# Kernel tuning notes

Measured on AMD Instinct MI355X. Metric: run time of the kernel, lower is better.

## Reference

```python
import jax, jax.numpy as jnp
import numpy as np

B, N, C = 8, 1024, 768      # batch, tokens, dim
H, HD = 8, 96               # num_heads (= top-k experts per token), head_dim
E, T = 24, 9                # num_experts, task_num
SCALE = HD ** -0.5
W_SWITCH, W_Z = 0.1, 0.001  # switchloss, zloss weights from __init__ defaults


def setup_inputs() -> dict:
    key = jax.random.key(0)
    ks = jax.random.split(key, 5)
    g = lambda k, sh, sc: jax.random.normal(k, sh, dtype=jnp.float32) * sc
    return {
        "x": g(ks[0], (B, N, C), 1.0),
        "W_gate": g(ks[1], (T, C, E), C ** -0.5),   # per-task gating weights
        "W_in": g(ks[2], (E, C, HD), C ** -0.5),    # expert q projections (TaskMoE.map)
        "W_out": g(ks[3], (E, HD, C), HD ** -0.5),  # expert output projections (TaskMoE.reduce)
        "W_kv": g(ks[4], (C, 2 * HD), C ** -0.5),   # shared kv_proj (MQA-style)
        "task_bh": 3,
    }


def reference(x, W_gate, W_in, W_out, W_kv, task_bh):
    # ---- task-conditioned top-k gating (eval path: no noise, no sampling) ----
    logits = jnp.einsum('bnc,ce->bne', x, W_gate[task_bh])          # [B,N,E]
    probs = jax.nn.softmax(logits, axis=-1)
    top_g, top_i = jax.lax.top_k(probs, H)                          # [B,N,H]
    top_g = top_g / (jnp.sum(top_g, axis=-1, keepdims=True) + 1e-6)
    # ---- TaskMoE.map: per-head q = selected expert projection of x ----
    q_all = jnp.einsum('bnc,ecd->bned', x, W_in)                    # [B,N,E,HD]
    q = jnp.take_along_axis(q_all, top_i[..., None], axis=2)        # [B,N,H,HD]
    # ---- shared K/V (single head) ----
    kv = x @ W_kv                                                   # [B,N,2*HD]
    k, v = kv[..., :HD], kv[..., HD:]
    # ---- MQA attention ----
    attn = jnp.einsum('bihd,bjd->bhij', q, k) * SCALE               # [B,H,N,N]
    attn = jax.nn.softmax(attn, axis=-1)
    o = jnp.einsum('bhij,bjd->bihd', attn, v)                       # [B,N,H,HD]
    # ---- TaskMoE.reduce: gate-weighted combine through output experts ----
    onehot = jax.nn.one_hot(top_i, E, dtype=o.dtype)                # [B,N,H,E]
    z = jnp.einsum('bnhd,bnhe,bnh->bned', o, onehot, top_g)         # [B,N,E,HD]
    out = jnp.einsum('bned,edc->bnc', z, W_out)                     # [B,N,C]
    # ---- auxiliary routing losses (switch load-balance + z-loss) ----
    importance = probs.mean(axis=(0, 1))                            # [E]
    load = onehot.sum(axis=2).mean(axis=(0, 1)) / H                 # [E]
    switchloss = E * jnp.sum(importance * load)
    zloss = jnp.mean(jax.nn.logsumexp(logits, axis=-1) ** 2)
    aux_loss = W_SWITCH * switchloss + W_Z * zloss
    return out, aux_loss
```

## Files before the change

kernel.cpp:

```cpp
#include <hip/hip_runtime.h>
#include <hip/hip_bf16.h>
#include <math.h>

#define BB 8
#define NN 1024
#define CC 768
#define HH 8
#define HD 96
#define EE 24
#define NT (BB*NN)
#define NSLOT (NT*HH)
#define EC (EE*HD)
#define CAPQ 8192
#define ASCALE 0.10206207261596575f
#define AL2 0.14724446f
#define DEFER_THR 11.5415603f

typedef unsigned short u16;
typedef unsigned char u8;
typedef unsigned int u32;
typedef unsigned long long u64;
typedef __attribute__((ext_vector_type(8))) short s16x8;
typedef __attribute__((ext_vector_type(4))) float f32x4;
typedef __attribute__((ext_vector_type(16))) float f32x16;

__device__ __forceinline__ u16 f2b(float f) {
  unsigned u = __builtin_bit_cast(unsigned, f);
  unsigned r = u + 0x7fffu + ((u >> 16) & 1u);
  return (u16)(r >> 16);
}

__device__ __forceinline__ float fexp2(float x) {
  float r; asm("v_exp_f32 %0, %1" : "=v"(r) : "v"(x)); return r;
}

__device__ __forceinline__ u32 cvtpk(float a, float b) {
  u32 d; asm("v_cvt_pk_bf16_f32 %0, %1, %2" : "=v"(d) : "v"(a), "v"(b)); return d;
}

__device__ __forceinline__ void gload16(const u16* g, u16* lds) {
  __builtin_amdgcn_global_load_lds(
      (const __attribute__((address_space(1))) void*)g,
      (__attribute__((address_space(3))) void*)lds, 16, 0, 0);
}

__device__ __forceinline__ int xcd_remap(int bid, int nwg) {
  int q = nwg >> 3, r = nwg & 7;
  int xcd = bid & 7, idx = bid >> 3;
  return (xcd < r ? xcd * (q + 1) : r * (q + 1) + (xcd - r) * q) + idx;
}

#define WS_CNT   0
#define WS_IMP   96
#define WS_ZSUM  192
#define WS_G     256
#define WS_EID   (WS_G + NSLOT*4)
#define WS_KVK   (WS_EID + NSLOT)
#define WS_VT    (WS_KVK + NT*128*2)
#define WS_WIN   (WS_VT + (size_t)96*NT*2)
#define WS_WOUT  (WS_WIN + (size_t)EC*CC*2)
#define WS_WKV   (WS_WOUT + (size_t)CC*EC*2)
#define WS_QA    (WS_WKV + 192*CC*2)
#define WS_Z     (WS_QA + (size_t)NT*EC*2)
#define WS_XB    WS_Z
#define WS_BUCKET (WS_Z + (size_t)16*1024*1024)

__global__ __launch_bounds__(256) void gate_kernel(
    const float* __restrict__ x, const float* __restrict__ Wg_all,
    const int* __restrict__ task_p, float* __restrict__ ws_f,
    int* __restrict__ ws_i, u8* __restrict__ eids, u16* __restrict__ xb,
    int* __restrict__ bucket)
{
  __shared__ float xs[64][65];
  __shared__ float wgs[64][24];
  __shared__ float lgt[64][26];
  __shared__ float zlo[64];
  __shared__ int hist[EE];
  __shared__ int gbase[EE];

  int t = threadIdx.x;
  int w = t >> 6, r = t & 63;
  int e0 = w * 6;
  int tok0 = blockIdx.x * 64;
  const float* Wg = Wg_all + (size_t)task_p[0] * CC * EE;

  if (t < EE) hist[t] = 0;

  float acc[6];
  #pragma unroll
  for (int c = 0; c < 6; c++) acc[c] = 0.f;

  for (int kb = 0; kb < CC; kb += 64) {
    __syncthreads();
    #pragma unroll
    for (int i = 0; i < 4; i++) {
      int idx = i * 256 + t;
      int rr = idx >> 4, cc = (idx & 15) << 2;
      float4 v = *(const float4*)&x[(size_t)(tok0 + rr) * CC + kb + cc];
      *(float4*)&xs[rr][cc] = v;
      u64 pk = (u64)f2b(v.x) | ((u64)f2b(v.y) << 16) |
               ((u64)f2b(v.z) << 32) | ((u64)f2b(v.w) << 48);
      *(u64*)&xb[(size_t)(tok0 + rr) * CC + kb + cc] = pk;
    }
    #pragma unroll
    for (int i = 0; i < 3; i++) {
      int idx = i * 256 + t;
      int kk = idx / 12, c2 = idx % 12;
      *(float2*)&wgs[kk][c2 * 2] = *(const float2*)&Wg[(size_t)(kb + kk) * EE + c2 * 2];
    }
    __syncthreads();
    #pragma unroll 16
    for (int k = 0; k < 64; k++) {
      float xv = xs[r][k];
      float2 w01 = *(const float2*)&wgs[k][e0];
      float2 w23 = *(const float2*)&wgs[k][e0 + 2];
      float2 w45 = *(const float2*)&wgs[k][e0 + 4];
      acc[0] += xv * w01.x; acc[1] += xv * w01.y;
      acc[2] += xv * w23.x; acc[3] += xv * w23.y;
      acc[4] += xv * w45.x; acc[5] += xv * w45.y;
    }
  }
  __syncthreads();
  #pragma unroll
  for (int c = 0; c < 6; c++) lgt[r][e0 + c] = acc[c];
  __syncthreads();

  int my_e[8], loc[8];
  if (t < 64) {
    int token = tok0 + t;
    float l[EE];
    #pragma unroll
    for (int e = 0; e < EE; e++) l[e] = lgt[t][e];
    float mx = l[0];
    #pragma unroll
    for (int e = 1; e < EE; e++) mx = fmaxf(mx, l[e]);
    float se = 0.f; float probs[EE];
    #pragma unroll
    for (int e = 0; e < EE; e++) { probs[e] = __expf(l[e] - mx); se += probs[e]; }
    float inv = 1.f / se;
    #pragma unroll
    for (int e = 0; e < EE; e++) probs[e] *= inv;
    float lse = mx + __logf(se);
    zlo[t] = lse * lse;

    unsigned taken = 0u;
    float gsum = 0.f;
    float my_g[8];
    #pragma unroll
    for (int h = 0; h < HH; h++) {
      float best = -1.f; int bi = 0;
      #pragma unroll
      for (int e = 0; e < EE; e++) {
        bool ok = !((taken >> e) & 1u) && (probs[e] > best);
        best = ok ? probs[e] : best;
        bi   = ok ? e : bi;
      }
      taken |= 1u << bi;
      gsum += best;
      my_g[h] = best; my_e[h] = bi;
    }
    float ginv = 1.f / (gsum + 1e-6f);
    float4 g0, g1;
    g0.x = my_g[0] * ginv; g0.y = my_g[1] * ginv; g0.z = my_g[2] * ginv; g0.w = my_g[3] * ginv;
    g1.x = my_g[4] * ginv; g1.y = my_g[5] * ginv; g1.z = my_g[6] * ginv; g1.w = my_g[7] * ginv;
    float* gbuf = ws_f + WS_G / 4;
    *(float4*)&gbuf[(size_t)token * HH]     = g0;
    *(float4*)&gbuf[(size_t)token * HH + 4] = g1;
    u64 pk = 0;
    #pragma unroll
    for (int h = 0; h < HH; h++) pk |= (u64)(u8)my_e[h] << (8 * h);
    *(u64*)&eids[(size_t)token * HH] = pk;
    #pragma unroll
    for (int h = 0; h < HH; h++) loc[h] = atomicAdd(&hist[my_e[h]], 1);
    #pragma unroll
    for (int e = 0; e < EE; e++) lgt[t][e] = probs[e];
  }
  __syncthreads();
  if (t < EE) {
    float s = 0.f;
    #pragma unroll 8
    for (int rr = 0; rr < 64; rr++) s += lgt[rr][t];
    atomicAdd(ws_f + WS_IMP / 4 + t, s);
    gbase[t] = atomicAdd(&ws_i[t], hist[t]);
  } else if (t == 32) {
    float s = 0.f;
    #pragma unroll 8
    for (int rr = 0; rr < 64; rr++) s += zlo[rr];
    atomicAdd(ws_f + WS_ZSUM / 4, s);
  }
  __syncthreads();
  if (t < 64) {
    int token = tok0 + t;
    #pragma unroll
    for (int h = 0; h < HH; h++)
      bucket[my_e[h] * CAPQ + gbase[my_e[h]] + loc[h]] = token;
  }
}

__global__ __launch_bounds__(256) void transpose_kernel(
    const float* __restrict__ src, u16* __restrict__ dst,
    int R, int C, int sB, int dR, int dB)
{
  __shared__ float tile[32][33];
  int e = blockIdx.z;
  const float* s = src + (size_t)e * sB;
  int t = threadIdx.x;
  int tr = t >> 5, tc = t & 31;
  #pragma unroll
  for (int i = 0; i < 4; i++) {
    int r = blockIdx.x * 32 + tr + i * 8;
    int c = blockIdx.y * 32 + tc;
    tile[tr + i * 8][tc] = s[(size_t)r * C + c];
  }
  __syncthreads();
  #pragma unroll
  for (int i = 0; i < 4; i++) {
    int sc = blockIdx.y * 32 + tr + i * 8;
    int sr = blockIdx.x * 32 + tc;
    dst[(size_t)e * dB + (size_t)sc * dR + sr] = f2b(tile[tc][tr + i * 8]);
  }
}

template<int BM, int BN, bool OUT_F32>
__global__ __launch_bounds__(256) void gemm_kernel(
    const u16* __restrict__ A, const u16* __restrict__ Bt,
    void* __restrict__ Cp, int M, int N, int K)
{
  constexpr int WM = BM / 2, WN = BN / 2;
  constexpr int FM = WM / 16, FN = WN / 16;
  __shared__ u16 As[BM][64];
  __shared__ u16 Bs[BN][64];
  int t = threadIdx.x;
  int w = t >> 6, l = t & 63;
  int lr = l & 15, lg = l >> 4;
  int wr = w >> 1, wc = w & 1;
  int nwg = gridDim.x * gridDim.y;
  int logical = xcd_remap(blockIdx.y * gridDim.x + blockIdx.x, nwg);
  int col0 = (logical % gridDim.x) * BN, row0 = (logical / gridDim.x) * BM;

  f32x4 acc[FM][FN];
  #pragma unroll
  for (int i = 0; i < FM; i++)
    #pragma unroll
    for (int j = 0; j < FN; j++) acc[i][j] = (f32x4)(0.f);

  int sr = t >> 3;
  int sc = t & 7;
  for (int kb = 0; kb < K; kb += 64) {
    __syncthreads();
    #pragma unroll
    for (int i = 0; i < BM / 32; i++) {
      int rr = i * 32 + sr;
      int ch = sc ^ (rr & 7);
      gload16(A + (size_t)(row0 + rr) * K + kb + ch * 8, &As[rr][sc * 8]);
    }
    #pragma unroll
    for (int i = 0; i < BN / 32; i++) {
      int rr = i * 32 + sr;
      int ch = sc ^ (rr & 7);
      gload16(Bt + (size_t)(col0 + rr) * K + kb + ch * 8, &Bs[rr][sc * 8]);
    }
    __syncthreads();
    #pragma unroll
    for (int ks = 0; ks < 2; ks++) {
      s16x8 af[FM], bf[FN];
      #pragma unroll
      for (int i = 0; i < FM; i++)
        af[i] = *(const s16x8*)&As[wr * WM + i * 16 + lr][8 * ((ks * 4 + lg) ^ (lr & 7))];
      #pragma unroll
      for (int j = 0; j < FN; j++)
        bf[j] = *(const s16x8*)&Bs[wc * WN + j * 16 + lr][8 * ((ks * 4 + lg) ^ (lr & 7))];
      #pragma unroll
      for (int i = 0; i < FM; i++)
        #pragma unroll
        for (int j = 0; j < FN; j++)
          acc[i][j] = __builtin_amdgcn_mfma_f32_16x16x32_bf16(af[i], bf[j], acc[i][j], 0, 0, 0);
    }
  }
  #pragma unroll
  for (int i = 0; i < FM; i++)
    #pragma unroll
    for (int j = 0; j < FN; j++)
      #pragma unroll
      for (int reg = 0; reg < 4; reg++) {
        int rr = row0 + wr * WM + i * 16 + lg * 4 + reg;
        int cc = col0 + wc * WN + j * 16 + lr;
        if (OUT_F32) ((float*)Cp)[(size_t)rr * N + cc] = acc[i][j][reg];
        else ((u16*)Cp)[(size_t)rr * N + cc] = f2b(acc[i][j][reg]);
      }
}

__global__ __launch_bounds__(256) void qproj_kernel(
    const u16* __restrict__ xb, const u16* __restrict__ winT,
    const int* __restrict__ ws_i, const int* __restrict__ bucket,
    u16* __restrict__ qall)
{
  int e = blockIdx.y;
  int t0 = blockIdx.x * 128;
  int cnt = ws_i[e];
  if (t0 >= cnt) return;
  __shared__ u16 As[128][64];
  __shared__ u16 Bs[96][64];
  __shared__ int tok_s[128];
  int t = threadIdx.x;
  if (t < 128) tok_s[t] = bucket[e * CAPQ + min(t0 + t, cnt - 1)];
  __syncthreads();
  int w = t >> 6, l = t & 63;
  int lr = l & 15, lg = l >> 4;
  int wr = w >> 1, wc = w & 1;
  const u16* Bt = winT + (size_t)e * HD * CC;

  f32x4 acc[4][3];
  #pragma unroll
  for (int i = 0; i < 4; i++)
    #pragma unroll
    for (int j = 0; j < 3; j++) acc[i][j] = (f32x4)(0.f);

  int sr = t >> 3, sc = t & 7;
  int atok[4];
  #pragma unroll
  for (int i = 0; i < 4; i++) atok[i] = tok_s[i * 32 + sr];

  for (int kb = 0; kb < CC; kb += 64) {
    __syncthreads();
    #pragma unroll
    for (int i = 0; i < 4; i++) {
      int rr = i * 32 + sr;
      int ch = sc ^ (rr & 7);
      gload16(xb + (size_t)atok[i] * CC + kb + ch * 8, &As[rr][sc * 8]);
    }
    #pragma unroll
    for (int i = 0; i < 3; i++) {
      int rr = i * 32 + sr;
      int ch = sc ^ (rr & 7);
      gload16(Bt + (size_t)rr * CC + kb + ch * 8, &Bs[rr][sc * 8]);
    }
    __syncthreads();
    #pragma unroll
    for (int ks = 0; ks < 2; ks++) {
      s16x8 af[4], bf[3];
      #pragma unroll
      for (int i = 0; i < 4; i++)
        af[i] = *(const s16x8*)&As[wr * 64 + i * 16 + lr][8 * ((ks * 4 + lg) ^ (lr & 7))];
      #pragma unroll
      for (int j = 0; j < 3; j++)
        bf[j] = *(const s16x8*)&Bs[wc * 48 + j * 16 + lr][8 * ((ks * 4 + lg) ^ (lr & 7))];
      #pragma unroll
      for (int i = 0; i < 4; i++)
        #pragma unroll
        for (int j = 0; j < 3; j++)
          acc[i][j] = __builtin_amdgcn_mfma_f32_16x16x32_bf16(af[i], bf[j], acc[i][j], 0, 0, 0);
    }
  }
  #pragma unroll
  for (int i = 0; i < 4; i++)
    #pragma unroll
    for (int reg = 0; reg < 4; reg++) {
      int rr = wr * 64 + i * 16 + lg * 4 + reg;
      if (t0 + rr < cnt) {
        int tok = tok_s[rr];
        u16* qp = qall + (size_t)tok * EC + e * HD + wc * 48;
        #pragma unroll
        for (int j = 0; j < 3; j++)
          qp[j * 16 + lr] = f2b(acc[i][j][reg]);
      }
    }
}

__global__ __launch_bounds__(256) void kvproj_kernel(
    const u16* __restrict__ xb, const u16* __restrict__ wkvT,
    u16* __restrict__ kvbk, u16* __restrict__ vtb)
{
  __shared__ u16 As[128][64];
  __shared__ u16 Bs[64][64];
  int t = threadIdx.x;
  int w = t >> 6, l = t & 63;
  int lr = l & 15, lg = l >> 4;
  int wr = w >> 1, wc = w & 1;
  int nwg = gridDim.x * gridDim.y;
  int logical = xcd_remap(blockIdx.y * gridDim.x + blockIdx.x, nwg);
  int col0 = (logical % gridDim.x) * 64, row0 = (logical / gridDim.x) * 128;

  f32x4 acc[4][2];
  #pragma unroll
  for (int i = 0; i < 4; i++)
    #pragma unroll
    for (int j = 0; j < 2; j++) acc[i][j] = (f32x4)(0.f);

  int sr = t >> 3, sc = t & 7;
  for (int kb = 0; kb < CC; kb += 64) {
    __syncthreads();
    #pragma unroll
    for (int i = 0; i < 4; i++) {
      int rr = i * 32 + sr;
      int ch = sc ^ (rr & 7);
      gload16(xb + (size_t)(row0 + rr) * CC + kb + ch * 8, &As[rr][sc * 8]);
    }
    #pragma unroll
    for (int i = 0; i < 2; i++) {
      int rr = i * 32 + sr;
      int ch = sc ^ (rr & 7);
      gload16(wkvT + (size_t)(col0 + rr) * CC + kb + ch * 8, &Bs[rr][sc * 8]);
    }
    __syncthreads();
    #pragma unroll
    for (int ks = 0; ks < 2; ks++) {
      s16x8 af[4], bf[2];
      #pragma unroll
      for (int i = 0; i < 4; i++)
        af[i] = *(const s16x8*)&As[wr * 64 + i * 16 + lr][8 * ((ks * 4 + lg) ^ (lr & 7))];
      #pragma unroll
      for (int j = 0; j < 2; j++)
        bf[j] = *(const s16x8*)&Bs[wc * 32 + j * 16 + lr][8 * ((ks * 4 + lg) ^ (lr & 7))];
      #pragma unroll
      for (int i = 0; i < 4; i++)
        #pragma unroll
        for (int j = 0; j < 2; j++)
          acc[i][j] = __builtin_amdgcn_mfma_f32_16x16x32_bf16(af[i], bf[j], acc[i][j], 0, 0, 0);
    }
  }
  #pragma unroll
  for (int i = 0; i < 4; i++)
    #pragma unroll
    for (int j = 0; j < 2; j++) {
      int cb = col0 + wc * 32 + j * 16 + lr;
      int rb = row0 + wr * 64 + i * 16 + lg * 4;
      if (cb < 96) {
        int ch = cb >> 3, ci = cb & 7;
        #pragma unroll
        for (int reg = 0; reg < 4; reg++) {
          int tok = rb + reg;
          kvbk[(size_t)tok * 128 + 8 * (ch ^ (tok & 7)) + ci] = f2b(acc[i][j][reg]);
        }
      } else {
        int d = cb - 96;
        u64 pk = (u64)f2b(acc[i][j][0]) | ((u64)f2b(acc[i][j][1]) << 16) |
                 ((u64)f2b(acc[i][j][2]) << 32) | ((u64)f2b(acc[i][j][3]) << 48);
        int blkbase = rb & ~63;
        int ch = (rb & 63) >> 3;
        *(u64*)&vtb[(size_t)d * NT + blkbase + 8 * (ch ^ (d & 7)) + (rb & 7)] = pk;
      }
    }
}

__global__ __launch_bounds__(256, 2) void attn_kernel(
    const u16* __restrict__ qall, const u16* __restrict__ kvbk,
    const u16* __restrict__ vtb, const u8* __restrict__ eids,
    const float* __restrict__ gbuf, u16* __restrict__ z)
{
  __shared__ u16 Ks[2][64][128];
  __shared__ u16 Vt[2][96][64];
  int b = blockIdx.y;
  int tok0 = blockIdx.x * 32;
  int t = threadIdx.x;
  int w = t >> 6, l = t & 63;
  int h = blockIdx.z * 4 + w;
  int lo = l & 31, hi = l >> 5;

  s16x8 qf[6];
  {
    int tok = b * NN + tok0 + lo;
    int e = eids[tok * HH + h];
    const u16* qp = qall + (size_t)tok * EC + e * HD + hi * 8;
    #pragma unroll
    for (int ks = 0; ks < 6; ks++)
      qf[ks] = *(const s16x8*)(qp + ks * 16);
  }

  const u16* kvwin = kvbk + (size_t)(b * NN) * 128;
  const u16* vwin  = vtb + (size_t)(b * NN);

  f32x16 o0 = (f32x16)(0.f), o1 = (f32x16)(0.f), o2 = (f32x16)(0.f);
  float m = -1e30f, lsum = 0.f;

  #pragma unroll
  for (int k2 = 0; k2 < 4; k2++) {
    int c = t + k2 * 256;
    gload16(kvwin + c * 8, &Ks[0][0][0] + c * 8);
  }
  #pragma unroll
  for (int k2 = 0; k2 < 3; k2++) {
    int c = t + k2 * 256;
    gload16(vwin + (size_t)(c >> 3) * NT + (c & 7) * 8, &Vt[0][0][0] + c * 8);
  }

  for (int jt = 0; jt < 16; jt++) {
    __syncthreads();
    if (jt < 15) {
      int j0 = (jt + 1) * 64;
      int nb = (jt + 1) & 1;
      const u16* kb_ = kvwin + (size_t)j0 * 128;
      #pragma unroll
      for (int k2 = 0; k2 < 4; k2++) {
        int c = t + k2 * 256;
        gload16(kb_ + c * 8, &Ks[nb][0][0] + c * 8);
      }
      const u16* vb_ = vwin + j0;
      #pragma unroll
      for (int k2 = 0; k2 < 3; k2++) {
        int c = t + k2 * 256;
        gload16(vb_ + (size_t)(c >> 3) * NT + (c & 7) * 8, &Vt[nb][0][0] + c * 8);
      }
    }
    int buf = jt & 1;

    f32x16 s0 = (f32x16)(0.f), s1 = (f32x16)(0.f);
    #pragma unroll
    for (int ks = 0; ks < 6; ks++) {
      int pos = 8 * ((2 * ks + hi) ^ (lo & 7));
      s16x8 a0 = *(const s16x8*)&Ks[buf][lo][pos];
      s16x8 a1 = *(const s16x8*)&Ks[buf][32 + lo][pos];
      s0 = __builtin_amdgcn_mfma_f32_32x32x16_bf16(a0, qf[ks], s0, 0, 0, 0);
      s1 = __builtin_amdgcn_mfma_f32_32x32x16_bf16(a1, qf[ks], s1, 0, 0, 0);
    }

    float pm = fmaxf(s0[0], s0[1]);
    #pragma unroll
    for (int rg = 2; rg < 16; rg += 2) pm = fmaxf(pm, fmaxf(s0[rg], s0[rg + 1]));
    #pragma unroll
    for (int rg = 0; rg < 16; rg += 2) pm = fmaxf(pm, fmaxf(s1[rg], s1[rg + 1]));
    pm = fmaxf(pm, __shfl_xor(pm, 32));
    pm *= AL2;

    if (!__all(pm - m <= DEFER_THR)) {
      float mn = fmaxf(m, pm);
      float al = fexp2(m - mn);
      m = mn; lsum *= al;
      #pragma unroll
      for (int rg = 0; rg < 16; rg++) {
        int qrow = (rg & 3) + 8 * (rg >> 2) + 4 * hi;
        float alr = __shfl(al, qrow);
        o0[rg] *= alr; o1[rg] *= alr; o2[rg] *= alr;
      }
    }

    float ts = 0.f;
    u32 wpk[2][4][2];
    #pragma unroll
    for (int kb2 = 0; kb2 < 2; kb2++)
      #pragma unroll
      for (int rr = 0; rr < 4; rr++)
        #pragma unroll
        for (int pp = 0; pp < 2; pp++) {
          float sA = kb2 ? s1[rr * 4 + 2 * pp]     : s0[rr * 4 + 2 * pp];
          float sB = kb2 ? s1[rr * 4 + 2 * pp + 1] : s0[rr * 4 + 2 * pp + 1];
          float eA = fexp2(fmaf(sA, AL2, -m));
          float eB = fexp2(fmaf(sB, AL2, -m));
          ts += eA + eB;
          wpk[kb2][rr][pp] = cvtpk(eA, eB);
        }
    lsum += ts;

    s16x8 pa[4];
    #pragma unroll
    for (int ks = 0; ks < 4; ks++) {
      int kb2 = ks >> 1;
      int rlo = (ks & 1) * 2, rhi = rlo + 1;
      u32 own_lo0 = wpk[kb2][rlo][0], own_lo1 = wpk[kb2][rlo][1];
      u32 own_hi0 = wpk[kb2][rhi][0], own_hi1 = wpk[kb2][rhi][1];
      u32 send0 = hi ? own_lo0 : own_hi0;
      u32 send1 = hi ? own_lo1 : own_hi1;
      u32 recv0 = (u32)__shfl_xor((int)send0, 32);
      u32 recv1 = (u32)__shfl_xor((int)send1, 32);
      union { s16x8 v; u32 u[4]; } pu;
      pu.u[0] = hi ? recv0 : own_lo0;
      pu.u[1] = hi ? recv1 : own_lo1;
      pu.u[2] = hi ? own_hi0 : recv0;
      pu.u[3] = hi ? own_hi1 : recv1;
      pa[ks] = pu.v;
    }

    #pragma unroll
    for (int ks = 0; ks < 4; ks++) {
      int pos = 8 * ((2 * ks + hi) ^ (lo & 7));
      s16x8 v0 = *(const s16x8*)&Vt[buf][lo][pos];
      s16x8 v1 = *(const s16x8*)&Vt[buf][32 + lo][pos];
      s16x8 v2 = *(const s16x8*)&Vt[buf][64 + lo][pos];
      o0 = __builtin_amdgcn_mfma_f32_32x32x16_bf16(pa[ks], v0, o0, 0, 0, 0);
      o1 = __builtin_amdgcn_mfma_f32_32x32x16_bf16(pa[ks], v1, o1, 0, 0, 0);
      o2 = __builtin_amdgcn_mfma_f32_32x32x16_bf16(pa[ks], v2, o2, 0, 0, 0);
    }
  }

  float lt = lsum + __shfl_xor(lsum, 32);
  #pragma unroll
  for (int rg = 0; rg < 16; rg++) {
    int qrow = (rg & 3) + 8 * (rg >> 2) + 4 * hi;
    float lv = __shfl(lt, qrow);
    int tok = b * NN + tok0 + qrow;
    int slot = tok * HH + h;
    float scl = gbuf[slot] / lv;
    int e = eids[slot];
    u16* zp = z + (size_t)tok * EC + e * HD + lo;
    zp[0]  = f2b(o0[rg] * scl);
    zp[32] = f2b(o1[rg] * scl);
    zp[64] = f2b(o2[rg] * scl);
  }
}

__global__ void aux_kernel(const float* __restrict__ ws_f,
                           const int* __restrict__ ws_i, float* __restrict__ out)
{
  if (threadIdx.x == 0 && blockIdx.x == 0) {
    float sw = 0.f;
    for (int e = 0; e < EE; e++) {
      float imp = ws_f[WS_IMP / 4 + e] / (float)NT;
      float load = (float)ws_i[e] / (float)(NT * HH);
      sw += imp * load;
    }
    float zl = ws_f[WS_ZSUM / 4] / (float)NT;
    out[(size_t)NT * CC] = 0.1f * ((float)EE * sw) + 0.001f * zl;
  }
}

extern "C" void kernel_launch(void* const* d_in, const int* in_sizes, int n_in,
                              void* d_out, int out_size, void* d_ws, size_t ws_size,
                              hipStream_t stream)
{
  const float* x    = (const float*)d_in[0];
  const float* Wg   = (const float*)d_in[1];
  const float* Win  = (const float*)d_in[2];
  const float* Wout = (const float*)d_in[3];
  const float* Wkv  = (const float*)d_in[4];
  const int*   task = (const int*)d_in[5];
  float* out = (float*)d_out;
  float* ws_f = (float*)d_ws;
  int*   ws_i = (int*)d_ws;
  u8*  eids = (u8*)((char*)d_ws + WS_EID);
  u16* kvbk = (u16*)((char*)d_ws + WS_KVK);
  u16* vtb  = (u16*)((char*)d_ws + WS_VT);
  u16* winT = (u16*)((char*)d_ws + WS_WIN);
  u16* woutT= (u16*)((char*)d_ws + WS_WOUT);
  u16* wkvT = (u16*)((char*)d_ws + WS_WKV);
  u16* qall = (u16*)((char*)d_ws + WS_QA);
  u16* z    = (u16*)((char*)d_ws + WS_Z);
  u16* xb   = (u16*)((char*)d_ws + WS_XB);
  int* bucket = (int*)((char*)d_ws + WS_BUCKET);

  hipMemsetAsync(d_ws, 0, 256, stream);

  transpose_kernel<<<dim3(CC/32, HD/32, EE), 256, 0, stream>>>(Win, winT, CC, HD, CC*HD, CC, HD*CC);
  transpose_kernel<<<dim3(HD/32, CC/32, EE), 256, 0, stream>>>(Wout, woutT, HD, CC, HD*CC, EC, HD);
  transpose_kernel<<<dim3(CC/32, 192/32, 1), 256, 0, stream>>>(Wkv, wkvT, CC, 192, 0, CC, 0);

  gate_kernel<<<NT / 64, 256, 0, stream>>>(x, Wg, task, ws_f, ws_i, eids, xb, bucket);

  kvproj_kernel<<<dim3(3, NT/128), 256, 0, stream>>>(xb, wkvT, kvbk, vtb);
  qproj_kernel<<<dim3(NT/128, EE), 256, 0, stream>>>(xb, winT, ws_i, bucket, qall);

  hipMemsetAsync(z, 0, (size_t)NT * EC * 2, stream);

  attn_kernel<<<dim3(NN/32, BB, 2), 256, 0, stream>>>(qall, kvbk, vtb, eids, ws_f + WS_G/4, z);

  gemm_kernel<128, 64, true><<<dim3(CC/64, NT/128), 256, 0, stream>>>(
      z, woutT, out, NT, CC, EC);

  aux_kernel<<<1, 64, 0, stream>>>(ws_f, ws_i, out);
}
```

Baseline: 185.5 us.

## Split gate kernel K-reduction across more threads with smaller token tiles

The gating kernel now uses 32 tokens per block with 512 threads instead of 64 tokens with 256. Each thread covers a quarter of every 64-wide K chunk, and the partial sums are combined with a cross-lane shuffle plus a shared-memory scratch add. The aim is to launch twice as many blocks with shorter serial FMA chains, so the small-grid gate stage gets more parallelism. In exchange it adds reduction overhead, more blocks doing global atomics, and more redundant loads of the gate weights per token.

```diff
diff --git a/kernel.cpp b/kernel.cpp
--- a/kernel.cpp
+++ b/kernel.cpp
@@ -65,23 +65,26 @@
 #define WS_XB    WS_Z
 #define WS_BUCKET (WS_Z + (size_t)16*1024*1024)
 
-__global__ __launch_bounds__(256) void gate_kernel(
+__global__ __launch_bounds__(512) void gate_kernel(
     const float* __restrict__ x, const float* __restrict__ Wg_all,
     const int* __restrict__ task_p, float* __restrict__ ws_f,
     int* __restrict__ ws_i, u8* __restrict__ eids, u16* __restrict__ xb,
     int* __restrict__ bucket)
 {
-  __shared__ float xs[64][65];
+  __shared__ float xs[32][65];
   __shared__ float wgs[64][24];
-  __shared__ float lgt[64][26];
-  __shared__ float zlo[64];
+  __shared__ float scr[4][32][6];
+  __shared__ float lgt[32][26];
+  __shared__ float zlo[32];
   __shared__ int hist[EE];
   __shared__ int gbase[EE];
 
   int t = threadIdx.x;
-  int w = t >> 6, r = t & 63;
-  int e0 = w * 6;
-  int tok0 = blockIdx.x * 64;
+  int w = t >> 6, l = t & 63;
+  int eg = w & 3, e0 = eg * 6;
+  int r = l & 31;
+  int q = ((w >> 2) << 1) | (l >> 5);
+  int tok0 = blockIdx.x * 32;
   const float* Wg = Wg_all + (size_t)task_p[0] * CC * EE;
 
   if (t < EE) hist[t] = 0;
@@ -92,10 +95,8 @@
 
   for (int kb = 0; kb < CC; kb += 64) {
     __syncthreads();
-    #pragma unroll
-    for (int i = 0; i < 4; i++) {
-      int idx = i * 256 + t;
-      int rr = idx >> 4, cc = (idx & 15) << 2;
+    {
+      int rr = t >> 4, cc = (t & 15) << 2;
       float4 v = *(const float4*)&x[(size_t)(tok0 + rr) * CC + kb + cc];
       *(float4*)&xs[rr][cc] = v;
       u64 pk = (u64)f2b(v.x) | ((u64)f2b(v.y) << 16) |
@@ -103,40 +104,51 @@
       *(u64*)&xb[(size_t)(tok0 + rr) * CC + kb + cc] = pk;
     }
     #pragma unroll
-    for (int i = 0; i < 3; i++) {
-      int idx = i * 256 + t;
-      int kk = idx / 12, c2 = idx % 12;
-      *(float2*)&wgs[kk][c2 * 2] = *(const float2*)&Wg[(size_t)(kb + kk) * EE + c2 * 2];
-    }
-    __syncthreads();
-    #pragma unroll 16
-    for (int k = 0; k < 64; k++) {
-      float xv = xs[r][k];
-      float2 w01 = *(const float2*)&wgs[k][e0];
-      float2 w23 = *(const float2*)&wgs[k][e0 + 2];
-      float2 w45 = *(const float2*)&wgs[k][e0 + 4];
+    for (int i = 0; i < 2; i++) {
+      int idx = i * 512 + t;
+      if (idx < 768) {
+        int kk = idx / 12, c2 = idx % 12;
+        *(float2*)&wgs[kk][c2 * 2] = *(const float2*)&Wg[(size_t)(kb + kk) * EE + c2 * 2];
+      }
+    }
+    __syncthreads();
+    int k0 = q * 16;
+    #pragma unroll
+    for (int k = 0; k < 16; k++) {
+      float xv = xs[r][k0 + k];
+      float2 w01 = *(const float2*)&wgs[k0 + k][e0];
+      float2 w23 = *(const float2*)&wgs[k0 + k][e0 + 2];
+      float2 w45 = *(const float2*)&wgs[k0 + k][e0 + 4];
       acc[0] += xv * w01.x; acc[1] += xv * w01.y;
       acc[2] += xv * w23.x; acc[3] += xv * w23.y;
       acc[4] += xv * w45.x; acc[5] += xv * w45.y;
     }
   }
+  #pragma unroll
+  for (int c = 0; c < 6; c++) acc[c] += __shfl_xor(acc[c], 32);
+  if (w >= 4 && l < 32) {
+    #pragma unroll
+    for (int c = 0; c < 6; c++) scr[eg][r][c] = acc[c];
+  }
   __syncthreads();
-  #pragma unroll
-  for (int c = 0; c < 6; c++) lgt[r][e0 + c] = acc[c];
+  if (w < 4 && l < 32) {
+    #pragma unroll
+    for (int c = 0; c < 6; c++) lgt[r][e0 + c] = acc[c] + scr[eg][r][c];
+  }
   __syncthreads();
 
   int my_e[8], loc[8];
-  if (t < 64) {
+  if (t < 32) {
     int token = tok0 + t;
-    float l[EE];
-    #pragma unroll
-    for (int e = 0; e < EE; e++) l[e] = lgt[t][e];
-    float mx = l[0];
-    #pragma unroll
-    for (int e = 1; e < EE; e++) mx = fmaxf(mx, l[e]);
+    float lg[EE];
+    #pragma unroll
+    for (int e = 0; e < EE; e++) lg[e] = lgt[t][e];
+    float mx = lg[0];
+    #pragma unroll
+    for (int e = 1; e < EE; e++) mx = fmaxf(mx, lg[e]);
     float se = 0.f; float probs[EE];
     #pragma unroll
-    for (int e = 0; e < EE; e++) { probs[e] = __expf(l[e] - mx); se += probs[e]; }
+    for (int e = 0; e < EE; e++) { probs[e] = __expf(lg[e] - mx); se += probs[e]; }
     float inv = 1.f / se;
     #pragma unroll
     for (int e = 0; e < EE; e++) probs[e] *= inv;
@@ -179,17 +191,17 @@
   if (t < EE) {
     float s = 0.f;
     #pragma unroll 8
-    for (int rr = 0; rr < 64; rr++) s += lgt[rr][t];
+    for (int rr = 0; rr < 32; rr++) s += lgt[rr][t];
     atomicAdd(ws_f + WS_IMP / 4 + t, s);
     gbase[t] = atomicAdd(&ws_i[t], hist[t]);
   } else if (t == 32) {
     float s = 0.f;
     #pragma unroll 8
-    for (int rr = 0; rr < 64; rr++) s += zlo[rr];
+    for (int rr = 0; rr < 32; rr++) s += zlo[rr];
     atomicAdd(ws_f + WS_ZSUM / 4, s);
   }
   __syncthreads();
-  if (t < 64) {
+  if (t < 32) {
     int token = tok0 + t;
     #pragma unroll
     for (int h = 0; h < HH; h++)
@@ -643,7 +655,7 @@
   transpose_kernel<<<dim3(HD/32, CC/32, EE), 256, 0, stream>>>(Wout, woutT, HD, CC, HD*CC, EC, HD);
   transpose_kernel<<<dim3(CC/32, 192/32, 1), 256, 0, stream>>>(Wkv, wkvT, CC, 192, 0, CC, 0);
 
-  gate_kernel<<<NT / 64, 256, 0, stream>>>(x, Wg, task, ws_f, ws_i, eids, xb, bucket);
+  gate_kernel<<<NT / 32, 512, 0, stream>>>(x, Wg, task, ws_f, ws_i, eids, xb, bucket);
 
   kvproj_kernel<<<dim3(3, NT/128), 256, 0, stream>>>(xb, wkvT, kvbk, vtb);
   qproj_kernel<<<dim3(NT/128, EE), 256, 0, stream>>>(xb, winT, ws_i, bucket, qall);
```

Result: faster. 178.8 us (-3.6%).
